# Performance work log

Hardware: AMD Instinct MI355X
Metric: run time of the kernel (lower is better)

## Reference

```python
import jax, jax.numpy as jnp
import numpy as np

NUM_HEADS = 8
DIM_HIDDEN = 512


def setup_inputs() -> dict:
    key = jax.random.key(0)
    k1, k2, k3, k4 = jax.random.split(key, 4)
    B, N, C = 4, 2048, DIM_HIDDEN
    x = jax.random.normal(k1, (B, N, C), dtype=jnp.float32)
    # proj_in: Linear(C, 3C, bias=False); stored as [in, out] for x @ W
    W_in = jax.random.normal(k2, (C, 3 * C), dtype=jnp.float32) * (1.0 / np.sqrt(C))
    # proj_out: Linear(C, C) with bias
    W_out = jax.random.normal(k3, (C, C), dtype=jnp.float32) * (1.0 / np.sqrt(C))
    b_out = jax.random.normal(k4, (C,), dtype=jnp.float32) * 0.01
    return {"x": x, "W_in": W_in, "W_out": W_out, "b_out": b_out}


def reference(x, W_in, W_out, b_out):
    B, N, C = x.shape
    H = NUM_HEADS
    D = C // H
    scale = D ** -0.5
    qkv = (x @ W_in).reshape(B, N, 3, H, D)
    qkv = jnp.transpose(qkv, (2, 0, 3, 1, 4))  # [3, B, H, N, D]
    q, k, v = qkv[0], qkv[1], qkv[2]
    attn = jnp.einsum("bhqd,bhkd->bhqk", q, k) * scale
    attn = jax.nn.softmax(attn, axis=-1)
    out = jnp.einsum("bhqk,bhkd->bhqd", attn, v)  # [B, H, N, D]
    out = jnp.transpose(out, (0, 2, 1, 3)).reshape(B, N, C)
    return out @ W_out + b_out
```

## Files before the change

kernel.cpp:

```cpp
#include <hip/hip_runtime.h>

typedef unsigned short u16;
typedef unsigned int   u32;
using s16x8 = __attribute__((ext_vector_type(8))) short;
using s16x4 = __attribute__((ext_vector_type(4))) short;
using f32x4 = __attribute__((ext_vector_type(4))) float;

#define NB   4
#define SEQ  2048
#define CH   512
#define NH   8
#define HD   64
#define C3   1536
#define LOG2E 1.44269504088896f

__device__ __forceinline__ u16 f2bf(float f) {
  u32 u = __float_as_uint(f);
  u32 r = u + 0x7fffu + ((u >> 16) & 1u);
  return (u16)(r >> 16);
}

__device__ __forceinline__ u32 cvtpk(float a, float b) {
  u32 r;
  asm("v_cvt_pk_bf16_f32 %0, %1, %2" : "=v"(r) : "v"(a), "v"(b));
  return r;
}

__device__ __forceinline__ float ex2(float x) {
#if __has_builtin(__builtin_amdgcn_exp2f)
  return __builtin_amdgcn_exp2f(x);
#else
  return exp2f(x);
#endif
}

#define GLL16(gp, lp) __builtin_amdgcn_global_load_lds( \
    (const __attribute__((address_space(1))) u32*)(gp), \
    (__attribute__((address_space(3))) u32*)(lp), 16, 0, 0)

__global__ __launch_bounds__(256) void conv_x(const float* __restrict__ in,
                                              u16* __restrict__ out, int n4) {
  int i = blockIdx.x * 256 + threadIdx.x;
  if (i >= n4) return;
  float4 v = ((const float4*)in)[i];
  u32 a = (u32)f2bf(v.x) | ((u32)f2bf(v.y) << 16);
  u32 b = (u32)f2bf(v.z) | ((u32)f2bf(v.w) << 16);
  ((uint2*)out)[i] = make_uint2(a, b);
}

__global__ __launch_bounds__(256) void conv_tr(const float* __restrict__ in,
                                               u16* __restrict__ out, int R, int C) {
  __shared__ float tb[64][68];
  const int c0 = blockIdx.x * 64, r0 = blockIdx.y * 64;
  const int t = threadIdx.x;
#pragma unroll
  for (int i = 0; i < 4; ++i) {
    int idx = i * 1024 + t * 4;
    int r = idx >> 6, c = idx & 63;
    float4 v = *(const float4*)(&in[(size_t)(r0 + r) * C + c0 + c]);
    tb[r][c] = v.x; tb[r][c + 1] = v.y; tb[r][c + 2] = v.z; tb[r][c + 3] = v.w;
  }
  __syncthreads();
  const int cc = t >> 2, rr0 = (t & 3) * 16;
  u16 tmp[16];
#pragma unroll
  for (int j = 0; j < 16; ++j) tmp[j] = f2bf(tb[rr0 + j][cc]);
#pragma unroll
  for (int j = 0; j < 4; ++j) {
    u32 a = (u32)tmp[4 * j] | ((u32)tmp[4 * j + 1] << 16);
    u32 b = (u32)tmp[4 * j + 2] | ((u32)tmp[4 * j + 3] << 16);
    *(uint2*)(&out[(size_t)(c0 + cc) * R + r0 + rr0 + 4 * j]) = make_uint2(a, b);
  }
}

template <int KTOT>
__device__ __forceinline__ void gemm_core(const u16* __restrict__ Ag,
                                          const u16* __restrict__ Bg,
                                          int m0, int n0, f32x4 (&acc)[4][4],
                                          u16* As, u16* Bs) {
  const int t = threadIdx.x;
  const int l = t & 63, w = t >> 6;
  const int wr = w >> 1, wc = w & 1;
  const int lo = l & 15, hi = l >> 4;
  const int srow_base = w * 8 + (l >> 3);
  const int scolb = (l & 7) * 16;

  for (int k0 = 0; k0 < KTOT; k0 += 64) {
    __syncthreads();
#pragma unroll
    for (int i = 0; i < 4; ++i) {
      int row = i * 32 + srow_base;
      int sw  = (row & 7) << 4;
      GLL16((const char*)Ag + (size_t)(m0 + row) * 1024 + k0 * 2 + (scolb ^ sw),
            (char*)As + row * 128 + scolb);
      GLL16((const char*)Bg + (size_t)(n0 + row) * 1024 + k0 * 2 + (scolb ^ sw),
            (char*)Bs + row * 128 + scolb);
    }
    __syncthreads();
#pragma unroll
    for (int s = 0; s < 2; ++s) {
      s16x8 af[4], bf[4];
#pragma unroll
      for (int mi = 0; mi < 4; ++mi) {
        int row = wr * 64 + mi * 16 + lo;
        af[mi] = *(const s16x8*)((const char*)As + row * 128 +
                                 ((s * 64 + hi * 16) ^ ((row & 7) << 4)));
      }
#pragma unroll
      for (int ni = 0; ni < 4; ++ni) {
        int row = wc * 64 + ni * 16 + lo;
        bf[ni] = *(const s16x8*)((const char*)Bs + row * 128 +
                                 ((s * 64 + hi * 16) ^ ((row & 7) << 4)));
      }
#pragma unroll
      for (int mi = 0; mi < 4; ++mi)
#pragma unroll
        for (int ni = 0; ni < 4; ++ni)
          acc[mi][ni] = __builtin_amdgcn_mfma_f32_16x16x32_bf16(af[mi], bf[ni],
                                                                acc[mi][ni], 0, 0, 0);
    }
  }
}

__global__ __launch_bounds__(256) void gemm_qkv(const u16* __restrict__ xb,
                                                const u16* __restrict__ WinT,
                                                u16* __restrict__ qb,
                                                u16* __restrict__ kb,
                                                u16* __restrict__ vb) {
  __shared__ __align__(16) u16 As[8192];
  __shared__ __align__(16) u16 Bs[8192];
  const int m0 = blockIdx.y * 128, n0 = blockIdx.x * 128;
  f32x4 acc[4][4];
#pragma unroll
  for (int i = 0; i < 4; ++i)
#pragma unroll
    for (int j = 0; j < 4; ++j) acc[i][j] = (f32x4){0.f, 0.f, 0.f, 0.f};

  gemm_core<CH>(xb, WinT, m0, n0, acc, As, Bs);

  const int t = threadIdx.x, l = t & 63, w = t >> 6;
  const int wr = w >> 1, wc = w & 1, lo = l & 15, hi = l >> 4;
#pragma unroll
  for (int ni = 0; ni < 4; ++ni) {
    const int n = n0 + wc * 64 + ni * 16 + lo;
    const int tq = n >> 9, h = (n >> 6) & 7, d = n & 63;
    u16* dst = (tq == 0) ? qb : ((tq == 1) ? kb : vb);
    const float sc = (tq == 0) ? 0.125f * LOG2E : 1.0f;
#pragma unroll
    for (int mi = 0; mi < 4; ++mi)
#pragma unroll
      for (int r = 0; r < 4; ++r) {
        const int m = m0 + wr * 64 + mi * 16 + hi * 4 + r;
        const int b = m >> 11, ns = m & (SEQ - 1);
        dst[((size_t)((b * NH + h) * SEQ + ns)) * HD + d] = f2bf(acc[mi][ni][r] * sc);
      }
  }
}

__global__ __launch_bounds__(512) void attn(const u16* __restrict__ qg,
                                            const u16* __restrict__ kg,
                                            const u16* __restrict__ vg,
                                            u16* __restrict__ ao) {
  __shared__ __align__(16) u16 Ks[4096];
  __shared__ __align__(16) u16 Vs[4096];
  __shared__ __align__(16) u16 Ps[8192];
  const int t = threadIdx.x, l = t & 63, w = t >> 6;
  const int lo = l & 15, hi = l >> 4;
  const int wg = blockIdx.x;
  const int L  = (wg & 7) * 64 + (wg >> 3);
  const int bh = L >> 4, qblk = L & 15;
  const int q0 = qblk * 128;
  const u16* qp = qg + (size_t)bh * SEQ * HD;
  const u16* kp = kg + (size_t)bh * SEQ * HD;
  const u16* vp = vg + (size_t)bh * SEQ * HD;

  s16x8 qf[2];
#pragma unroll
  for (int s = 0; s < 2; ++s)
    qf[s] = *(const s16x8*)(qp + (size_t)(q0 + w * 16 + lo) * HD + s * 32 + hi * 8);

  f32x4 oacc[4];
#pragma unroll
  for (int i = 0; i < 4; ++i) oacc[i] = (f32x4){0.f, 0.f, 0.f, 0.f};
  float m_s = -1e30f, l_s = 0.f;

  u16* Pw = Ps + w * 1024;
  const int vkv = (t & 31) * 2, vd0 = (t >> 5) * 4;
  const int krow = t >> 3, kcolb = (t & 7) * 16;
  const int swl = (lo & 7) << 4;

  for (int kt = 0; kt < SEQ; kt += 64) {
    __syncthreads();
    GLL16((const char*)kp + (size_t)(kt + krow) * 128 + (kcolb ^ ((krow & 7) << 4)),
          (char*)Ks + t * 16);
    {
      s16x4 v0 = *(const s16x4*)(vp + (size_t)(kt + vkv) * HD + vd0);
      s16x4 v1 = *(const s16x4*)(vp + (size_t)(kt + vkv + 1) * HD + vd0);
#pragma unroll
      for (int j = 0; j < 4; ++j) {
        int d = vd0 + j;
        u32 pw = (u32)(u16)v0[j] | ((u32)(u16)v1[j] << 16);
        *(u32*)((char*)Vs + ((d * 128 + vkv * 2) ^ ((d & 7) << 4))) = pw;
      }
    }
    __syncthreads();

    f32x4 st[4];
#pragma unroll
    for (int i = 0; i < 4; ++i) st[i] = (f32x4){0.f, 0.f, 0.f, 0.f};
    __builtin_amdgcn_s_setprio(1);
#pragma unroll
    for (int s = 0; s < 2; ++s)
#pragma unroll
      for (int ct = 0; ct < 4; ++ct) {
        int row = ct * 16 + lo;
        s16x8 kf = *(const s16x8*)((const char*)Ks + row * 128 +
                                   ((s * 64 + hi * 16) ^ ((row & 7) << 4)));
        st[ct] = __builtin_amdgcn_mfma_f32_16x16x32_bf16(kf, qf[s], st[ct], 0, 0, 0);
      }
    __builtin_amdgcn_s_setprio(0);

    float a0 = fmaxf(fmaxf(st[0][0], st[1][0]), fmaxf(st[2][0], st[3][0]));
    float a1 = fmaxf(fmaxf(st[0][1], st[1][1]), fmaxf(st[2][1], st[3][1]));
    float a2 = fmaxf(fmaxf(st[0][2], st[1][2]), fmaxf(st[2][2], st[3][2]));
    float a3 = fmaxf(fmaxf(st[0][3], st[1][3]), fmaxf(st[2][3], st[3][3]));
    float mx = fmaxf(fmaxf(a0, a1), fmaxf(a2, a3));
    mx = fmaxf(mx, __shfl_xor(mx, 16));
    mx = fmaxf(mx, __shfl_xor(mx, 32));
    const float mn = fmaxf(m_s, mx);
    const float rs = ex2(m_s - mn);
    m_s = mn;
    float psum[4];
#pragma unroll
    for (int ct = 0; ct < 4; ++ct) {
      float p0 = ex2(st[ct][0] - mn), p1 = ex2(st[ct][1] - mn);
      float p2 = ex2(st[ct][2] - mn), p3 = ex2(st[ct][3] - mn);
      st[ct][0] = p0; st[ct][1] = p1; st[ct][2] = p2; st[ct][3] = p3;
      psum[ct] = (p0 + p1) + (p2 + p3);
    }
    float sum = (psum[0] + psum[1]) + (psum[2] + psum[3]);
    sum += __shfl_xor(sum, 16);
    sum += __shfl_xor(sum, 32);
    l_s = l_s * rs + sum;

#pragma unroll
    for (int ct = 0; ct < 4; ++ct) {
      u32 pk0 = cvtpk(st[ct][0], st[ct][1]);
      u32 pk1 = cvtpk(st[ct][2], st[ct][3]);
      *(uint2*)((char*)Pw + ((lo * 128 + ct * 32 + hi * 8) ^ swl)) =
          make_uint2(pk0, pk1);
    }
#pragma unroll
    for (int ct = 0; ct < 4; ++ct) {
      oacc[ct][0] *= rs; oacc[ct][1] *= rs;
      oacc[ct][2] *= rs; oacc[ct][3] *= rs;
    }

    s16x8 pf[2];
#pragma unroll
    for (int s = 0; s < 2; ++s)
      pf[s] = *(const s16x8*)((const char*)Pw + ((lo * 128 + s * 64 + hi * 16) ^ swl));
    __builtin_amdgcn_s_setprio(1);
#pragma unroll
    for (int s = 0; s < 2; ++s)
#pragma unroll
      for (int ct = 0; ct < 4; ++ct) {
        int row = ct * 16 + lo;
        s16x8 vt = *(const s16x8*)((const char*)Vs + row * 128 +
                                   ((s * 64 + hi * 16) ^ ((row & 7) << 4)));
        oacc[ct] = __builtin_amdgcn_mfma_f32_16x16x32_bf16(vt, pf[s], oacc[ct], 0, 0, 0);
      }
    __builtin_amdgcn_s_setprio(0);
  }

  const int b = bh >> 3, h = bh & 7;
  const float inv = 1.0f / l_s;
  u16* aop = ao + ((size_t)(b * SEQ) + q0 + w * 16 + lo) * CH + h * HD;
#pragma unroll
  for (int ct = 0; ct < 4; ++ct) {
    u32 o0 = cvtpk(oacc[ct][0] * inv, oacc[ct][1] * inv);
    u32 o1 = cvtpk(oacc[ct][2] * inv, oacc[ct][3] * inv);
    *(uint2*)(aop + ct * 16 + hi * 4) = make_uint2(o0, o1);
  }
}

__global__ __launch_bounds__(256) void gemm_out(const u16* __restrict__ ao,
                                                const u16* __restrict__ WoutT,
                                                const float* __restrict__ bias,
                                                float* __restrict__ out) {
  __shared__ __align__(16) u16 As[8192];
  __shared__ __align__(16) u16 Bs[8192];
  const int m0 = blockIdx.y * 128, n0 = blockIdx.x * 128;
  f32x4 acc[4][4];
#pragma unroll
  for (int i = 0; i < 4; ++i)
#pragma unroll
    for (int j = 0; j < 4; ++j) acc[i][j] = (f32x4){0.f, 0.f, 0.f, 0.f};

  gemm_core<CH>(ao, WoutT, m0, n0, acc, As, Bs);

  const int t = threadIdx.x, l = t & 63, w = t >> 6;
  const int wr = w >> 1, wc = w & 1, lo = l & 15, hi = l >> 4;
#pragma unroll
  for (int ni = 0; ni < 4; ++ni) {
    const int n = n0 + wc * 64 + ni * 16 + lo;
    const float bv = bias[n];
#pragma unroll
    for (int mi = 0; mi < 4; ++mi)
#pragma unroll
      for (int r = 0; r < 4; ++r) {
        const int m = m0 + wr * 64 + mi * 16 + hi * 4 + r;
        out[(size_t)m * CH + n] = acc[mi][ni][r] + bv;
      }
  }
}

extern "C" void kernel_launch(void* const* d_in, const int* in_sizes, int n_in,
                              void* d_out, int out_size, void* d_ws, size_t ws_size,
                              hipStream_t stream) {
  const float* x    = (const float*)d_in[0];
  const float* Win  = (const float*)d_in[1];
  const float* Wout = (const float*)d_in[2];
  const float* bout = (const float*)d_in[3];
  float* out = (float*)d_out;
  char* ws = (char*)d_ws;

  const size_t MB = 1u << 20;
  u16* xb    = (u16*)(ws);
  u16* WinT  = (u16*)(ws + 8 * MB);
  u16* WoutT = (u16*)(ws + 10 * MB);
  u16* qb    = (u16*)(ws + 12 * MB);
  u16* kb    = (u16*)(ws + 20 * MB);
  u16* vb    = (u16*)(ws + 28 * MB);
  u16* ao    = (u16*)(ws + 36 * MB);

  conv_x<<<4096, 256, 0, stream>>>(x, xb, (NB * SEQ * CH) / 4);
  conv_tr<<<dim3(C3 / 64, CH / 64), 256, 0, stream>>>(Win, WinT, CH, C3);
  conv_tr<<<dim3(CH / 64, CH / 64), 256, 0, stream>>>(Wout, WoutT, CH, CH);

  gemm_qkv<<<dim3(C3 / 128, (NB * SEQ) / 128), 256, 0, stream>>>(xb, WinT, qb, kb, vb);
  attn<<<512, 512, 0, stream>>>(qb, kb, vb, ao);
  gemm_out<<<dim3(CH / 128, (NB * SEQ) / 128), 256, 0, stream>>>(ao, WoutT, bout, out);
}
```

Baseline: 119.0 us.

## Double-buffer K/V tiles in attention and skip softmax rescale when max is stable

Switches the attention kernel's K and V shared-memory tiles to double buffers. The next tile's K async load and V global reads are issued before the current tile's MFMAs, and one barrier per iteration replaces two. It also adds a lazy online-softmax rescale: the running max and the accumulator scaling are updated only when some lane's new max exceeds the old one by more than 8 (log2 units). This removes the exp and multiply work in most iterations, at the cost of more LDS use and some risk of reduced precision from values up to 2^8 above the reference max.

```diff
diff --git a/kernel.cpp b/kernel.cpp
--- a/kernel.cpp
+++ b/kernel.cpp
@@ -161,8 +161,8 @@
                                             const u16* __restrict__ kg,
                                             const u16* __restrict__ vg,
                                             u16* __restrict__ ao) {
-  __shared__ __align__(16) u16 Ks[4096];
-  __shared__ __align__(16) u16 Vs[4096];
+  __shared__ __align__(16) u16 Ks[2][4096];
+  __shared__ __align__(16) u16 Vs[2][4096];
   __shared__ __align__(16) u16 Ps[8192];
   const int t = threadIdx.x, l = t & 63, w = t >> 6;
   const int lo = l & 15, hi = l >> 4;
@@ -186,24 +186,30 @@
 
   u16* Pw = Ps + w * 1024;
   const int vkv = (t & 31) * 2, vd0 = (t >> 5) * 4;
-  const int krow = t >> 3, kcolb = (t & 7) * 16;
+  const int ksrc = (t >> 3) * 128 + (((t & 7) * 16) ^ (((t >> 3) & 7) << 4));
   const int swl = (lo & 7) << 4;
 
-  for (int kt = 0; kt < SEQ; kt += 64) {
-    __syncthreads();
-    GLL16((const char*)kp + (size_t)(kt + krow) * 128 + (kcolb ^ ((krow & 7) << 4)),
-          (char*)Ks + t * 16);
-    {
-      s16x4 v0 = *(const s16x4*)(vp + (size_t)(kt + vkv) * HD + vd0);
-      s16x4 v1 = *(const s16x4*)(vp + (size_t)(kt + vkv + 1) * HD + vd0);
-#pragma unroll
-      for (int j = 0; j < 4; ++j) {
-        int d = vd0 + j;
-        u32 pw = (u32)(u16)v0[j] | ((u32)(u16)v1[j] << 16);
-        *(u32*)((char*)Vs + ((d * 128 + vkv * 2) ^ ((d & 7) << 4))) = pw;
-      }
-    }
-    __syncthreads();
+  GLL16((const char*)kp + ksrc, (char*)&Ks[0][0] + t * 16);
+  s16x4 vr0 = *(const s16x4*)(vp + (size_t)vkv * HD + vd0);
+  s16x4 vr1 = *(const s16x4*)(vp + (size_t)(vkv + 1) * HD + vd0);
+#pragma unroll
+  for (int j = 0; j < 4; ++j) {
+    int d = vd0 + j;
+    u32 pw = (u32)(u16)vr0[j] | ((u32)(u16)vr1[j] << 16);
+    *(u32*)((char*)&Vs[0][0] + ((d * 128 + vkv * 2) ^ ((d & 7) << 4))) = pw;
+  }
+  __syncthreads();
+
+  for (int it = 0; it < 32; ++it) {
+    const int cur = it & 1, nxt = cur ^ 1;
+    const u16* Kc = &Ks[cur][0];
+    const u16* Vc = &Vs[cur][0];
+    if (it < 31) {
+      const size_t nb = (size_t)(it + 1) * 64;
+      GLL16((const char*)(kp + nb * HD) + ksrc, (char*)&Ks[nxt][0] + t * 16);
+      vr0 = *(const s16x4*)(vp + (nb + vkv) * HD + vd0);
+      vr1 = *(const s16x4*)(vp + (nb + vkv + 1) * HD + vd0);
+    }
 
     f32x4 st[4];
 #pragma unroll
@@ -214,7 +220,7 @@
 #pragma unroll
       for (int ct = 0; ct < 4; ++ct) {
         int row = ct * 16 + lo;
-        s16x8 kf = *(const s16x8*)((const char*)Ks + row * 128 +
+        s16x8 kf = *(const s16x8*)((const char*)Kc + row * 128 +
                                    ((s * 64 + hi * 16) ^ ((row & 7) << 4)));
         st[ct] = __builtin_amdgcn_mfma_f32_16x16x32_bf16(kf, qf[s], st[ct], 0, 0, 0);
       }
@@ -227,21 +233,29 @@
     float mx = fmaxf(fmaxf(a0, a1), fmaxf(a2, a3));
     mx = fmaxf(mx, __shfl_xor(mx, 16));
     mx = fmaxf(mx, __shfl_xor(mx, 32));
-    const float mn = fmaxf(m_s, mx);
-    const float rs = ex2(m_s - mn);
-    m_s = mn;
+    if (__any(mx > m_s + 8.0f)) {
+      const float mn = fmaxf(m_s, mx);
+      const float rs = ex2(m_s - mn);
+      m_s = mn;
+      l_s *= rs;
+#pragma unroll
+      for (int ct = 0; ct < 4; ++ct) {
+        oacc[ct][0] *= rs; oacc[ct][1] *= rs;
+        oacc[ct][2] *= rs; oacc[ct][3] *= rs;
+      }
+    }
     float psum[4];
 #pragma unroll
     for (int ct = 0; ct < 4; ++ct) {
-      float p0 = ex2(st[ct][0] - mn), p1 = ex2(st[ct][1] - mn);
-      float p2 = ex2(st[ct][2] - mn), p3 = ex2(st[ct][3] - mn);
+      float p0 = ex2(st[ct][0] - m_s), p1 = ex2(st[ct][1] - m_s);
+      float p2 = ex2(st[ct][2] - m_s), p3 = ex2(st[ct][3] - m_s);
       st[ct][0] = p0; st[ct][1] = p1; st[ct][2] = p2; st[ct][3] = p3;
       psum[ct] = (p0 + p1) + (p2 + p3);
     }
     float sum = (psum[0] + psum[1]) + (psum[2] + psum[3]);
     sum += __shfl_xor(sum, 16);
     sum += __shfl_xor(sum, 32);
-    l_s = l_s * rs + sum;
+    l_s += sum;
 
 #pragma unroll
     for (int ct = 0; ct < 4; ++ct) {
@@ -250,11 +264,6 @@
       *(uint2*)((char*)Pw + ((lo * 128 + ct * 32 + hi * 8) ^ swl)) =
           make_uint2(pk0, pk1);
     }
-#pragma unroll
-    for (int ct = 0; ct < 4; ++ct) {
-      oacc[ct][0] *= rs; oacc[ct][1] *= rs;
-      oacc[ct][2] *= rs; oacc[ct][3] *= rs;
-    }
 
     s16x8 pf[2];
 #pragma unroll
@@ -266,11 +275,23 @@
 #pragma unroll
       for (int ct = 0; ct < 4; ++ct) {
         int row = ct * 16 + lo;
-        s16x8 vt = *(const s16x8*)((const char*)Vs + row * 128 +
+        s16x8 vt = *(const s16x8*)((const char*)Vc + row * 128 +
                                    ((s * 64 + hi * 16) ^ ((row & 7) << 4)));
         oacc[ct] = __builtin_amdgcn_mfma_f32_16x16x32_bf16(vt, pf[s], oacc[ct], 0, 0, 0);
       }
     __builtin_amdgcn_s_setprio(0);
+
+    if (it < 31) {
+#pragma unroll
+      for (int j = 0; j < 4; ++j) {
+        int d = vd0 + j;
+        u32 pw = (u32)(u16)vr0[j] | ((u32)(u16)vr1[j] << 16);
+        *(u32*)((char*)&Vs[nxt][0] + ((d * 128 + vkv * 2) ^ ((d & 7) << 4))) = pw;
+      }
+      asm volatile("s_waitcnt vmcnt(0) lgkmcnt(0)" ::: "memory");
+      __builtin_amdgcn_s_barrier();
+      __builtin_amdgcn_sched_barrier(0);
+    }
   }
 
   const int b = bh >> 3, h = bh & 7;
```

Measured after the change: 109.6 us. 1.09x faster.
